# Optimization experiments

Measured on AMD Instinct MI355X. Metric: run time of the kernel, lower is better.

## Reference

```python
import jax, jax.numpy as jnp
import numpy as np
from jax.scipy.linalg import solve_triangular

N = 2          # n_assets
EPS = 1e-10    # jitter added to Sigma_bar and cov
B = 4_000_000  # batch of states


def setup_inputs() -> dict:
    key = jax.random.key(0)
    ks = jax.random.split(key, 10)
    x = jax.random.normal(ks[0], (B,), jnp.float32)
    omega = jax.random.normal(ks[1], (1,), jnp.float32)
    p = jax.random.uniform(ks[2], (B,), jnp.float32, minval=0.01, maxval=0.99)
    dlnf_dp = jax.random.normal(ks[3], (B,), jnp.float32)
    f = jax.random.uniform(ks[4], (B,), jnp.float32, minval=0.5, maxval=1.5)
    mu1 = 0.1 * jax.random.normal(ks[5], (N,), jnp.float32)
    mu2 = 0.1 * jax.random.normal(ks[6], (N,), jnp.float32)
    A1 = 0.1 * jax.random.normal(ks[7], (N, N), jnp.float32)
    Sigma1 = A1 @ A1.T + 0.05 * jnp.eye(N, dtype=jnp.float32)  # SPD
    A2 = 0.1 * jax.random.normal(ks[8], (N, N), jnp.float32)
    Sigma2 = A2 @ A2.T + 0.05 * jnp.eye(N, dtype=jnp.float32)  # SPD
    phi = 0.1 * jax.random.normal(ks[9], (N, 2), jnp.float32)
    cov_tril_unconstrained = jnp.eye(N, dtype=jnp.float32)
    return dict(x=x, omega=omega, p=p, dlnf_dp=dlnf_dp, f=f,
                mu1=mu1, mu2=mu2, Sigma1=Sigma1, Sigma2=Sigma2,
                phi=phi, cov_tril_unconstrained=cov_tril_unconstrained,
                Lambda=1, r=0)


def reference(x, omega, p, dlnf_dp, f, mu1, mu2, Sigma1, Sigma2,
              phi, cov_tril_unconstrained, Lambda, r):
    eye = jnp.eye(N, dtype=x.dtype)
    rr = jnp.asarray(r, x.dtype)
    lam = jnp.asarray(Lambda, x.dtype)

    # posterior moments
    pc = p[:, None]                                   # [B,1]
    mu_bar = pc * mu1[None, :] + (1.0 - pc) * mu2[None, :]   # [B,N]
    excess_mu = mu_bar - rr
    pm = p[:, None, None]                             # [B,1,1]
    Sigma_bar = pm * Sigma1[None] + (1.0 - pm) * Sigma2[None] + EPS * eye  # [B,N,N]

    chol = jnp.linalg.cholesky(Sigma_bar)             # lower, [B,N,N]
    U = jnp.swapaxes(chol, -1, -2)                    # upper (chol^T)

    # mean: -(x - omega) * (sigma^T)^-1 signal
    adj = p - dlnf_dp * p * (1.0 - p)                 # [B]
    signal = phi[:, 0][None, :] * (adj[:, None] * excess_mu) \
           + phi[:, 1][None, :] * excess_mu           # [B,N]
    sti = solve_triangular(U, signal[..., None], lower=False)[..., 0]  # [B,N]
    mean = -(x - omega)[:, None] * sti                # [B,N]

    # SPD core from unconstrained tril (exp on diagonal)
    raw = jnp.tril(cov_tril_unconstrained)
    d = jnp.diagonal(raw)
    tril = raw - jnp.diag(d) + jnp.diag(jnp.exp(d))
    spd_core = tril @ tril.T                          # [N,N]

    # cov = 0.5 * Lambda * f * (sigma^T)^-1 spd_core (sigma^-1)
    inv_U = solve_triangular(U, jnp.broadcast_to(eye, Sigma_bar.shape), lower=False)  # [B,N,N]
    cov = 0.5 * lam * f[:, None, None] * jnp.einsum('bij,jk,blk->bil', inv_U, spd_core, inv_U)
    cov = 0.5 * (cov + jnp.swapaxes(cov, -1, -2)) + EPS * eye
    return mean, cov
```

## Files before the change

### kernel.cpp

```cpp
#include <hip/hip_runtime.h>

#define EPS 1e-10f

__device__ __forceinline__ void compute_one(
    float xe, float pe, float de, float fe,
    float omega, float lam, float r,
    float mu10, float mu11, float mu20, float mu21,
    float s1a, float s1b, float s1c,
    float s2a, float s2b, float s2c,
    float phi00, float phi01, float phi10, float phi11,
    float sp00, float sp01, float sp11,
    float* m, float* c)
{
    float om = 1.0f - pe;

    float a  = pe * s1a + om * s2a + EPS;
    float b  = pe * s1b + om * s2b;
    float cc = pe * s1c + om * s2c + EPS;

    float l00 = sqrtf(a);
    float l10 = b / l00;
    float l11 = sqrtf(cc - l10 * l10);
    float inv_l00 = 1.0f / l00;
    float inv_l11 = 1.0f / l11;

    float mb0 = pe * mu10 + om * mu20 - r;
    float mb1 = pe * mu11 + om * mu21 - r;

    float adj  = pe - de * pe * om;
    float sig0 = mb0 * (phi00 * adj + phi01);
    float sig1 = mb1 * (phi10 * adj + phi11);

    float sti1 = sig1 * inv_l11;
    float sti0 = (sig0 - l10 * sti1) * inv_l00;

    float nxo = omega - xe;
    m[0] = nxo * sti0;
    m[1] = nxo * sti1;

    float iu00 = inv_l00;
    float iu11 = inv_l11;
    float iu01 = -(l10 * inv_l00) * inv_l11;

    float M00 = iu00 * sp00 + iu01 * sp01;
    float M01 = iu00 * sp01 + iu01 * sp11;
    float M10 = iu11 * sp01;
    float M11 = iu11 * sp11;
    float C00 = M00 * iu00 + M01 * iu01;
    float C01 = M01 * iu11;
    float C10 = M10 * iu00 + M11 * iu01;
    float C11 = M11 * iu11;

    float scale = 0.5f * lam * fe;
    float off = 0.5f * (scale * C01 + scale * C10);
    c[0] = scale * C00 + EPS;
    c[1] = off;
    c[2] = off;
    c[3] = scale * C11 + EPS;
}

__global__ __launch_bounds__(256) void poemv_kernel(
    const float* __restrict__ x, const float* __restrict__ omega_p,
    const float* __restrict__ p, const float* __restrict__ dlnf_dp,
    const float* __restrict__ f,
    const float* __restrict__ mu1, const float* __restrict__ mu2,
    const float* __restrict__ S1, const float* __restrict__ S2,
    const float* __restrict__ phi, const float* __restrict__ ct,
    const int* __restrict__ lambda_p, const int* __restrict__ r_p,
    float* __restrict__ out_mean, float* __restrict__ out_cov, int B)
{
    int tid = blockIdx.x * blockDim.x + threadIdx.x;
    int b0 = tid * 4;
    if (b0 >= B) return;

    float omega = omega_p[0];
    float lam   = (float)lambda_p[0];
    float r     = (float)r_p[0];
    float mu10 = mu1[0], mu11 = mu1[1];
    float mu20 = mu2[0], mu21 = mu2[1];
    float s1a = S1[0], s1b = S1[2], s1c = S1[3];
    float s2a = S2[0], s2b = S2[2], s2c = S2[3];
    float phi00 = phi[0], phi01 = phi[1], phi10 = phi[2], phi11 = phi[3];

    float e0 = expf(ct[0]);
    float e1 = expf(ct[3]);
    float t10 = ct[2];
    float sp00 = e0 * e0;
    float sp01 = t10 * e0;
    float sp11 = t10 * t10 + e1 * e1;

    if (b0 + 3 < B) {
        float4 xv = ((const float4*)x)[tid];
        float4 pv = ((const float4*)p)[tid];
        float4 dv = ((const float4*)dlnf_dp)[tid];
        float4 fv = ((const float4*)f)[tid];

        float m[8];
        float c[16];
        compute_one(xv.x, pv.x, dv.x, fv.x, omega, lam, r, mu10, mu11, mu20, mu21,
                    s1a, s1b, s1c, s2a, s2b, s2c, phi00, phi01, phi10, phi11,
                    sp00, sp01, sp11, m + 0, c + 0);
        compute_one(xv.y, pv.y, dv.y, fv.y, omega, lam, r, mu10, mu11, mu20, mu21,
                    s1a, s1b, s1c, s2a, s2b, s2c, phi00, phi01, phi10, phi11,
                    sp00, sp01, sp11, m + 2, c + 4);
        compute_one(xv.z, pv.z, dv.z, fv.z, omega, lam, r, mu10, mu11, mu20, mu21,
                    s1a, s1b, s1c, s2a, s2b, s2c, phi00, phi01, phi10, phi11,
                    sp00, sp01, sp11, m + 4, c + 8);
        compute_one(xv.w, pv.w, dv.w, fv.w, omega, lam, r, mu10, mu11, mu20, mu21,
                    s1a, s1b, s1c, s2a, s2b, s2c, phi00, phi01, phi10, phi11,
                    sp00, sp01, sp11, m + 6, c + 12);

        float4* mo = (float4*)(out_mean + (size_t)b0 * 2);
        mo[0] = make_float4(m[0], m[1], m[2], m[3]);
        mo[1] = make_float4(m[4], m[5], m[6], m[7]);
        float4* co = (float4*)(out_cov + (size_t)b0 * 4);
        co[0] = make_float4(c[0],  c[1],  c[2],  c[3]);
        co[1] = make_float4(c[4],  c[5],  c[6],  c[7]);
        co[2] = make_float4(c[8],  c[9],  c[10], c[11]);
        co[3] = make_float4(c[12], c[13], c[14], c[15]);
    } else {
        for (int b = b0; b < B; ++b) {
            float m[2], c[4];
            compute_one(x[b], p[b], dlnf_dp[b], f[b], omega, lam, r,
                        mu10, mu11, mu20, mu21, s1a, s1b, s1c, s2a, s2b, s2c,
                        phi00, phi01, phi10, phi11, sp00, sp01, sp11, m, c);
            out_mean[(size_t)b * 2 + 0] = m[0];
            out_mean[(size_t)b * 2 + 1] = m[1];
            out_cov[(size_t)b * 4 + 0] = c[0];
            out_cov[(size_t)b * 4 + 1] = c[1];
            out_cov[(size_t)b * 4 + 2] = c[2];
            out_cov[(size_t)b * 4 + 3] = c[3];
        }
    }
}

extern "C" void kernel_launch(void* const* d_in, const int* in_sizes, int n_in,
                              void* d_out, int out_size, void* d_ws, size_t ws_size,
                              hipStream_t stream) {
    const float* x     = (const float*)d_in[0];
    const float* omega = (const float*)d_in[1];
    const float* p     = (const float*)d_in[2];
    const float* dlnf  = (const float*)d_in[3];
    const float* f     = (const float*)d_in[4];
    const float* mu1   = (const float*)d_in[5];
    const float* mu2   = (const float*)d_in[6];
    const float* S1    = (const float*)d_in[7];
    const float* S2    = (const float*)d_in[8];
    const float* phi   = (const float*)d_in[9];
    const float* ct    = (const float*)d_in[10];
    const int*   lam   = (const int*)d_in[11];
    const int*   r     = (const int*)d_in[12];

    int B = in_sizes[0];
    float* out_mean = (float*)d_out;
    float* out_cov  = out_mean + (size_t)B * 2;

    int n4 = (B + 3) / 4;
    int threads = 256;
    int blocks = (n4 + threads - 1) / threads;
    poemv_kernel<<<blocks, threads, 0, stream>>>(
        x, omega, p, dlnf, f, mu1, mu2, S1, S2, phi, ct, lam, r,
        out_mean, out_cov, B);
}
```

Before: 185.1 us.

## Use 8 elements per thread, nontemporal stores, rsq intrinsics and precombined params

Each thread now handles 8 batch elements instead of 4, which halves the thread count and doubles the per-thread vector loads. Output writes go through nontemporal stores to reduce cache pollution on a streaming, write-heavy kernel. The Cholesky math uses hardware reciprocal square root and FMAs, and the constant differences (S1-S2, mu1-mu2) are folded once per thread. The rsq intrinsic has lower precision than sqrt plus divide, and there are fewer waves available to hide memory latency.

```diff
diff --git a/kernel.cpp b/kernel.cpp
--- a/kernel.cpp
+++ b/kernel.cpp
@@ -2,61 +2,89 @@
 
 #define EPS 1e-10f
 
+typedef float v4f __attribute__((ext_vector_type(4)));
+
+struct Params {
+    float omega, r, half_lam;
+    float mu20r, mu21r, dmu0, dmu1;
+    float s2a, s2b, s2c, da, db, dc;
+    float phi00, phi01, phi10, phi11;
+    float sp00, sp01, sp11;
+};
+
 __device__ __forceinline__ void compute_one(
-    float xe, float pe, float de, float fe,
-    float omega, float lam, float r,
-    float mu10, float mu11, float mu20, float mu21,
-    float s1a, float s1b, float s1c,
-    float s2a, float s2b, float s2c,
-    float phi00, float phi01, float phi10, float phi11,
-    float sp00, float sp01, float sp11,
-    float* m, float* c)
+    float xe, float pe, float de, float fe, const Params& P,
+    float& m0, float& m1, v4f& cv)
 {
     float om = 1.0f - pe;
 
-    float a  = pe * s1a + om * s2a + EPS;
-    float b  = pe * s1b + om * s2b;
-    float cc = pe * s1c + om * s2c + EPS;
+    float a  = fmaf(pe, P.da, P.s2a) + EPS;
+    float b  = fmaf(pe, P.db, P.s2b);
+    float cc = fmaf(pe, P.dc, P.s2c) + EPS;
 
-    float l00 = sqrtf(a);
-    float l10 = b / l00;
-    float l11 = sqrtf(cc - l10 * l10);
-    float inv_l00 = 1.0f / l00;
-    float inv_l11 = 1.0f / l11;
+    float inv_l00 = __builtin_amdgcn_rsqf(a);
+    float t       = b * inv_l00;
+    float dd      = fmaf(-t, t, cc);
+    float inv_l11 = __builtin_amdgcn_rsqf(dd);
 
-    float mb0 = pe * mu10 + om * mu20 - r;
-    float mb1 = pe * mu11 + om * mu21 - r;
+    float mb0 = fmaf(pe, P.dmu0, P.mu20r);
+    float mb1 = fmaf(pe, P.dmu1, P.mu21r);
 
-    float adj  = pe - de * pe * om;
-    float sig0 = mb0 * (phi00 * adj + phi01);
-    float sig1 = mb1 * (phi10 * adj + phi11);
+    float adj  = pe * fmaf(-de, om, 1.0f);
+    float sig0 = mb0 * fmaf(P.phi00, adj, P.phi01);
+    float sig1 = mb1 * fmaf(P.phi10, adj, P.phi11);
 
     float sti1 = sig1 * inv_l11;
-    float sti0 = (sig0 - l10 * sti1) * inv_l00;
+    float sti0 = fmaf(-t, sti1, sig0) * inv_l00;
 
-    float nxo = omega - xe;
-    m[0] = nxo * sti0;
-    m[1] = nxo * sti1;
+    float nxo = P.omega - xe;
+    m0 = nxo * sti0;
+    m1 = nxo * sti1;
 
     float iu00 = inv_l00;
     float iu11 = inv_l11;
-    float iu01 = -(l10 * inv_l00) * inv_l11;
+    float iu01 = -(t * inv_l00) * inv_l11;
 
-    float M00 = iu00 * sp00 + iu01 * sp01;
-    float M01 = iu00 * sp01 + iu01 * sp11;
-    float M10 = iu11 * sp01;
-    float M11 = iu11 * sp11;
-    float C00 = M00 * iu00 + M01 * iu01;
+    float M00 = fmaf(iu00, P.sp00, iu01 * P.sp01);
+    float M01 = fmaf(iu00, P.sp01, iu01 * P.sp11);
+    float M10 = iu11 * P.sp01;
+    float M11 = iu11 * P.sp11;
+    float C00 = fmaf(M00, iu00, M01 * iu01);
     float C01 = M01 * iu11;
-    float C10 = M10 * iu00 + M11 * iu01;
+    float C10 = fmaf(M10, iu00, M11 * iu01);
     float C11 = M11 * iu11;
 
-    float scale = 0.5f * lam * fe;
-    float off = 0.5f * (scale * C01 + scale * C10);
-    c[0] = scale * C00 + EPS;
-    c[1] = off;
-    c[2] = off;
-    c[3] = scale * C11 + EPS;
+    float scale = P.half_lam * fe;
+    float off   = 0.5f * scale * (C01 + C10);
+    cv.x = fmaf(scale, C00, EPS);
+    cv.y = off;
+    cv.z = off;
+    cv.w = fmaf(scale, C11, EPS);
+}
+
+__device__ __forceinline__ Params load_params(
+    const float* omega_p, const float* mu1, const float* mu2,
+    const float* S1, const float* S2, const float* phi, const float* ct,
+    const int* lambda_p, const int* r_p)
+{
+    Params P;
+    P.omega    = omega_p[0];
+    float lam  = (float)lambda_p[0];
+    P.half_lam = 0.5f * lam;
+    P.r        = (float)r_p[0];
+    float mu10 = mu1[0], mu11 = mu1[1], mu20 = mu2[0], mu21 = mu2[1];
+    P.mu20r = mu20 - P.r;  P.mu21r = mu21 - P.r;
+    P.dmu0  = mu10 - mu20; P.dmu1  = mu11 - mu21;
+    P.s2a = S2[0]; P.s2b = S2[2]; P.s2c = S2[3];
+    P.da  = S1[0] - P.s2a; P.db = S1[2] - P.s2b; P.dc = S1[3] - P.s2c;
+    P.phi00 = phi[0]; P.phi01 = phi[1]; P.phi10 = phi[2]; P.phi11 = phi[3];
+    float e0 = expf(ct[0]);
+    float e1 = expf(ct[3]);
+    float t10 = ct[2];
+    P.sp00 = e0 * e0;
+    P.sp01 = t10 * e0;
+    P.sp11 = fmaf(t10, t10, e1 * e1);
+    return P;
 }
 
 __global__ __launch_bounds__(256) void poemv_kernel(
@@ -70,66 +98,48 @@
     float* __restrict__ out_mean, float* __restrict__ out_cov, int B)
 {
     int tid = blockIdx.x * blockDim.x + threadIdx.x;
-    int b0 = tid * 4;
+    long b0 = (long)tid * 8;
     if (b0 >= B) return;
 
-    float omega = omega_p[0];
-    float lam   = (float)lambda_p[0];
-    float r     = (float)r_p[0];
-    float mu10 = mu1[0], mu11 = mu1[1];
-    float mu20 = mu2[0], mu21 = mu2[1];
-    float s1a = S1[0], s1b = S1[2], s1c = S1[3];
-    float s2a = S2[0], s2b = S2[2], s2c = S2[3];
-    float phi00 = phi[0], phi01 = phi[1], phi10 = phi[2], phi11 = phi[3];
+    Params P = load_params(omega_p, mu1, mu2, S1, S2, phi, ct, lambda_p, r_p);
 
-    float e0 = expf(ct[0]);
-    float e1 = expf(ct[3]);
-    float t10 = ct[2];
-    float sp00 = e0 * e0;
-    float sp01 = t10 * e0;
-    float sp11 = t10 * t10 + e1 * e1;
+    if (b0 + 7 < B) {
+        const v4f* x4 = (const v4f*)x;
+        const v4f* p4 = (const v4f*)p;
+        const v4f* d4 = (const v4f*)dlnf_dp;
+        const v4f* f4 = (const v4f*)f;
+        int q = tid * 2;
+        v4f xa = x4[q],     xb = x4[q + 1];
+        v4f pa = p4[q],     pb = p4[q + 1];
+        v4f da = d4[q],     db = d4[q + 1];
+        v4f fa = f4[q],     fb = f4[q + 1];
 
-    if (b0 + 3 < B) {
-        float4 xv = ((const float4*)x)[tid];
-        float4 pv = ((const float4*)p)[tid];
-        float4 dv = ((const float4*)dlnf_dp)[tid];
-        float4 fv = ((const float4*)f)[tid];
+        float xs[8] = {xa.x, xa.y, xa.z, xa.w, xb.x, xb.y, xb.z, xb.w};
+        float ps[8] = {pa.x, pa.y, pa.z, pa.w, pb.x, pb.y, pb.z, pb.w};
+        float ds[8] = {da.x, da.y, da.z, da.w, db.x, db.y, db.z, db.w};
+        float fs[8] = {fa.x, fa.y, fa.z, fa.w, fb.x, fb.y, fb.z, fb.w};
 
-        float m[8];
-        float c[16];
-        compute_one(xv.x, pv.x, dv.x, fv.x, omega, lam, r, mu10, mu11, mu20, mu21,
-                    s1a, s1b, s1c, s2a, s2b, s2c, phi00, phi01, phi10, phi11,
-                    sp00, sp01, sp11, m + 0, c + 0);
-        compute_one(xv.y, pv.y, dv.y, fv.y, omega, lam, r, mu10, mu11, mu20, mu21,
-                    s1a, s1b, s1c, s2a, s2b, s2c, phi00, phi01, phi10, phi11,
-                    sp00, sp01, sp11, m + 2, c + 4);
-        compute_one(xv.z, pv.z, dv.z, fv.z, omega, lam, r, mu10, mu11, mu20, mu21,
-                    s1a, s1b, s1c, s2a, s2b, s2c, phi00, phi01, phi10, phi11,
-                    sp00, sp01, sp11, m + 4, c + 8);
-        compute_one(xv.w, pv.w, dv.w, fv.w, omega, lam, r, mu10, mu11, mu20, mu21,
-                    s1a, s1b, s1c, s2a, s2b, s2c, phi00, phi01, phi10, phi11,
-                    sp00, sp01, sp11, m + 6, c + 12);
+        v4f* mo = (v4f*)(out_mean + b0 * 2);
+        v4f* co = (v4f*)(out_cov  + b0 * 4);
 
-        float4* mo = (float4*)(out_mean + (size_t)b0 * 2);
-        mo[0] = make_float4(m[0], m[1], m[2], m[3]);
-        mo[1] = make_float4(m[4], m[5], m[6], m[7]);
-        float4* co = (float4*)(out_cov + (size_t)b0 * 4);
-        co[0] = make_float4(c[0],  c[1],  c[2],  c[3]);
-        co[1] = make_float4(c[4],  c[5],  c[6],  c[7]);
-        co[2] = make_float4(c[8],  c[9],  c[10], c[11]);
-        co[3] = make_float4(c[12], c[13], c[14], c[15]);
+        #pragma unroll
+        for (int k = 0; k < 4; ++k) {
+            float m0, m1, m2, m3;
+            v4f c0, c1;
+            compute_one(xs[2*k],   ps[2*k],   ds[2*k],   fs[2*k],   P, m0, m1, c0);
+            compute_one(xs[2*k+1], ps[2*k+1], ds[2*k+1], fs[2*k+1], P, m2, m3, c1);
+            v4f mv = {m0, m1, m2, m3};
+            __builtin_nontemporal_store(mv, mo + k);
+            __builtin_nontemporal_store(c0, co + 2*k);
+            __builtin_nontemporal_store(c1, co + 2*k + 1);
+        }
     } else {
-        for (int b = b0; b < B; ++b) {
-            float m[2], c[4];
-            compute_one(x[b], p[b], dlnf_dp[b], f[b], omega, lam, r,
-                        mu10, mu11, mu20, mu21, s1a, s1b, s1c, s2a, s2b, s2c,
-                        phi00, phi01, phi10, phi11, sp00, sp01, sp11, m, c);
-            out_mean[(size_t)b * 2 + 0] = m[0];
-            out_mean[(size_t)b * 2 + 1] = m[1];
-            out_cov[(size_t)b * 4 + 0] = c[0];
-            out_cov[(size_t)b * 4 + 1] = c[1];
-            out_cov[(size_t)b * 4 + 2] = c[2];
-            out_cov[(size_t)b * 4 + 3] = c[3];
+        for (long b = b0; b < B; ++b) {
+            float m0, m1; v4f cv;
+            compute_one(x[b], p[b], dlnf_dp[b], f[b], P, m0, m1, cv);
+            out_mean[b * 2 + 0] = m0;
+            out_mean[b * 2 + 1] = m1;
+            ((v4f*)out_cov)[b] = cv;
         }
     }
 }
@@ -155,9 +165,9 @@
     float* out_mean = (float*)d_out;
     float* out_cov  = out_mean + (size_t)B * 2;
 
-    int n4 = (B + 3) / 4;
     int threads = 256;
-    int blocks = (n4 + threads - 1) / threads;
+    long n_thr = ((long)B + 7) / 8;
+    int blocks = (int)((n_thr + threads - 1) / threads);
     poemv_kernel<<<blocks, threads, 0, stream>>>(
         x, omega, p, dlnf, f, mu1, mu2, S1, S2, phi, ct, lam, r,
         out_mean, out_cov, B);
```

Measured after the change: 337.7 us. 1.82x slower.
